# Optimization experiments

Measured on AMD Instinct MI355X. Metric: run time of the kernel, lower is better.

The kernel has to match this reference:

```python
import jax, jax.numpy as jnp
import numpy as np

DIM = 768
H = 12
D = DIM // H  # head_dim = 64
SCALE = D ** -0.5


def _split_heads(x):
    # [b, n, h*d] -> [b, h, n, d]
    b, n, _ = x.shape
    return x.reshape(b, n, H, D).transpose(0, 2, 1, 3)


def setup_inputs() -> dict:
    key = jax.random.key(0)
    ks = jax.random.split(key, 16)
    B, NQ, NKV = 2, 2048, 2048
    w_init = lambda k: jax.random.normal(k, (DIM, DIM), dtype=jnp.float32) * 0.02
    return {
        "words": jax.random.normal(ks[0], (B, NQ, DIM), dtype=jnp.float32),
        "position_words": jax.random.normal(ks[1], (B, NQ, DIM), dtype=jnp.float32),
        "conscious_words": jax.random.normal(ks[2], (B, NQ, DIM), dtype=jnp.float32),
        "cross_kv": jax.random.normal(ks[3], (B, NKV, DIM), dtype=jnp.float32),
        "position_cross": jax.random.normal(ks[4], (B, NKV, DIM), dtype=jnp.float32),
        "Wq_w": w_init(ks[5]), "Wk_w": w_init(ks[6]), "Wv_w": w_init(ks[7]),
        "Wq_p": w_init(ks[8]), "Wk_p": w_init(ks[9]),
        "Wq_c": w_init(ks[10]), "Wk_c": w_init(ks[11]),
        "latent_k": jax.random.normal(ks[12], (DIM,), dtype=jnp.float32),
        "Wo": w_init(ks[13]),
        "bo": jnp.zeros((DIM,), dtype=jnp.float32),
    }


def reference(words, position_words, conscious_words, cross_kv, position_cross,
              Wq_w, Wk_w, Wv_w, Wq_p, Wk_p, Wq_c, Wk_c, latent_k, Wo, bo):
    # Queries from three sources. Sum of the 9 pairwise QK^T scores equals
    # (sum of Qs) @ (sum of Ks)^T by bilinearity of matmul (same math as source).
    q = _split_heads(words @ Wq_w) + _split_heads(position_words @ Wq_p) \
        + _split_heads(conscious_words @ Wq_c)        # [b,h,nq,d]
    # latent conscious key: same vector for every kv position
    kc = (latent_k @ Wk_c).reshape(H, D)              # [h,d]
    k = _split_heads(cross_kv @ Wk_w) + _split_heads(position_cross @ Wk_p) \
        + kc[None, :, None, :]                        # [b,h,nkv,d]
    v = _split_heads(cross_kv @ Wv_w)                 # [b,h,nkv,d]

    score = jnp.einsum('bhid,bhjd->bhij', q, k) * SCALE  # [b,h,nq,nkv]
    attn = jax.nn.softmax(score, axis=-1)
    out = jnp.einsum('bhij,bhjd->bhid', attn, v)      # [b,h,nq,d]
    b, _, nq, _ = out.shape
    out = out.transpose(0, 2, 1, 3).reshape(b, nq, H * D)
    return out @ Wo + bo
```

## Files before the change

### kernel.cpp

```cpp
#include <hip/hip_runtime.h>
#include <math.h>

#define DIM  768
#define NH   12
#define HD   64
#define NQ   2048
#define NKV  2048
#define QSC_LOG2E 0.18033688011112042f

typedef short bf16x8  __attribute__((ext_vector_type(8)));
typedef float f32x4   __attribute__((ext_vector_type(4)));
typedef float f32x16  __attribute__((ext_vector_type(16)));

__device__ __forceinline__ unsigned short f2bf(float f) {
    unsigned u = __float_as_uint(f);
    unsigned r = (u + 0x7FFFu + ((u >> 16) & 1u)) >> 16;
    return (unsigned short)r;
}
__device__ __forceinline__ float bf2f(unsigned short u) {
    return __uint_as_float(((unsigned)u) << 16);
}

__device__ __forceinline__ unsigned cvtpk_bf16(float a, float b) {
    unsigned r;
    asm("v_cvt_pk_bf16_f32 %0, %1, %2" : "=v"(r) : "v"(a), "v"(b));
    return r;
}

__device__ __forceinline__ void plswap(unsigned& a, unsigned& b) {
    asm("v_permlane32_swap_b32 %0, %1" : "+v"(a), "+v"(b));
}

__device__ __forceinline__ float vexp2f(float x) {
#if __has_builtin(__builtin_amdgcn_exp2f)
    return __builtin_amdgcn_exp2f(x);
#else
    float r;
    asm("v_exp_f32 %0, %1\ns_nop 0" : "=v"(r) : "v"(x));
    return r;
#endif
}

__device__ __forceinline__ void ld_lds16(void* lds, const void* g) {
    __builtin_amdgcn_global_load_lds(
        (const __attribute__((address_space(1))) unsigned int*)g,
        (__attribute__((address_space(3))) unsigned int*)lds, 16, 0, 0);
}

__device__ __forceinline__ f32x16 z16() {
    f32x16 r;
    #pragma unroll
    for (int e = 0; e < 16; ++e) r[e] = 0.f;
    return r;
}

union PB16 { unsigned u[4]; bf16x8 v; };

__global__ __launch_bounds__(256)
void prep_kernel(const float* __restrict__ w0, const float* __restrict__ w1,
                 const float* __restrict__ w2, const float* __restrict__ w3,
                 const float* __restrict__ w4, const float* __restrict__ w5,
                 const float* __restrict__ w6, unsigned short* __restrict__ wt,
                 const float* __restrict__ latent, const float* __restrict__ Wkc,
                 float* __restrict__ kc) {
    __shared__ float t[32][33];
    int bid = blockIdx.x;
    if (bid < 4032) {
        int iz = bid / 576, rem = bid - iz * 576;
        int iy = rem / 24, ix = rem - iy * 24;
        const float* Ws[7] = {w0, w1, w2, w3, w4, w5, w6};
        const float* W = Ws[iz];
        unsigned short* D = wt + (size_t)iz * (768 * 768);
        int r0 = iy * 32, c0 = ix * 32;
        int tx = threadIdx.x & 31, ty = threadIdx.x >> 5;
        #pragma unroll
        for (int yy = 0; yy < 4; ++yy)
            t[ty * 4 + yy][tx] = W[(size_t)(r0 + ty * 4 + yy) * 768 + c0 + tx];
        __syncthreads();
        #pragma unroll
        for (int yy = 0; yy < 4; ++yy)
            D[(size_t)(c0 + ty * 4 + yy) * 768 + r0 + tx] = f2bf(t[tx][ty * 4 + yy]);
    } else {
        int jb = bid - 4032;
        float (&red)[16][17] = *reinterpret_cast<float(*)[16][17]>(&t[0][0]);
        int tx = threadIdx.x & 15, ty = threadIdx.x >> 4;
        int j = jb * 16 + tx;
        float acc = 0.f;
        for (int i = ty * 48; i < ty * 48 + 48; ++i)
            acc += latent[i] * Wkc[i * DIM + j];
        red[ty][tx] = acc;
        __syncthreads();
        if (ty == 0) {
            float s = 0.f;
            #pragma unroll
            for (int k = 0; k < 16; ++k) s += red[k][tx];
            kc[j] = s;
        }
    }
}

struct QCfg {
    const float* A0; const float* A1; const float* A2;
    const unsigned short* B0; const unsigned short* B1; const unsigned short* B2;
    const float* bias; float scale; void* out; int npair; int mode;
};

__global__ __launch_bounds__(256)
void gemm_qvk(QCfg c0, QCfg c1, QCfg c2) {
    __shared__ unsigned short As[2][64 * 64];
    __shared__ unsigned short Bs[2][128 * 64];
    const int tid = threadIdx.x;
    const int w = tid >> 6, l = tid & 63, g = l >> 4, r16 = l & 15;

    int p = blockIdx.x;
    int xcd = p & 7, s = p >> 3;
    int bx = s % 6, gg = s / 6;
    int gidx = gg * 8 + xcd;
    int by = gidx & 63, z = gidx >> 6;
    const int n0 = bx * 128, m0 = by * 64;

    QCfg c = (z == 0) ? c0 : (z == 1) ? c1 : c2;
    const float* Alist[3] = {c.A0, c.A1, c.A2};
    const unsigned short* Blist[3] = {c.B0, c.B1, c.B2};

    const int ar = tid >> 2, ac = (tid & 3) * 16;
    const int aswz = (ar & 7) << 4;
    float4 av0, av1, av2, av3;

    f32x4 acc[4][2];
    #pragma unroll
    for (int i = 0; i < 4; ++i)
        #pragma unroll
        for (int j = 0; j < 2; ++j) acc[i][j] = (f32x4){0.f, 0.f, 0.f, 0.f};

#define ALOAD(AP, K0) { \
    const float* _ap = (AP) + (size_t)(m0 + ar) * 768 + (K0) + ac; \
    av0 = *(const float4*)_ap;       av1 = *(const float4*)(_ap + 4); \
    av2 = *(const float4*)(_ap + 8); av3 = *(const float4*)(_ap + 12); }

#define AWRITE(BUFI) { \
    uint4 u0_, u1_; \
    u0_.x = cvtpk_bf16(av0.x, av0.y); u0_.y = cvtpk_bf16(av0.z, av0.w); \
    u0_.z = cvtpk_bf16(av1.x, av1.y); u0_.w = cvtpk_bf16(av1.z, av1.w); \
    u1_.x = cvtpk_bf16(av2.x, av2.y); u1_.y = cvtpk_bf16(av2.z, av2.w); \
    u1_.z = cvtpk_bf16(av3.x, av3.y); u1_.w = cvtpk_bf16(av3.z, av3.w); \
    *(uint4*)((char*)As[BUFI] + ar * 128 + ((2 * ac) ^ aswz)) = u0_; \
    *(uint4*)((char*)As[BUFI] + ar * 128 + ((2 * ac + 16) ^ aswz)) = u1_; }

#define BSTAGE(BUFI, BP, K0) { _Pragma("unroll") \
    for (int is = 0; is < 4; ++is) { \
        int u = is * 256 + tid, r = u >> 3, cc = u & 7; \
        int col = ((cc ^ (r & 7)) << 3); \
        ld_lds16((char*)Bs[BUFI] + is * 4096 + w * 1024, \
                 (BP) + (size_t)(n0 + r) * 768 + (K0) + col); } }

    const int NSTEPS = c.npair * 12;
    int pn = 0, kn = 0;
    ALOAD(Alist[0], 0);
    BSTAGE(0, Blist[0], 0);
    AWRITE(0);
    kn = 64;
    __syncthreads();

    #pragma unroll 1
    for (int st = 0; st < NSTEPS; ++st) {
        int cur = st & 1;
        bool pre = (st + 1 < NSTEPS);
        if (pre) {
            ALOAD(Alist[pn], kn);
            BSTAGE(cur ^ 1, Blist[pn], kn);
        }
        const char* Ab = (const char*)As[cur];
        const char* Bb = (const char*)Bs[cur];
        #pragma unroll
        for (int kk = 0; kk < 2; ++kk) {
            bf16x8 af[4], bf[2];
            #pragma unroll
            for (int i = 0; i < 4; ++i) {
                int row = i * 16 + r16;
                af[i] = *(const bf16x8*)(Ab + row * 128 +
                          ((kk * 64 + g * 16) ^ ((row & 7) << 4)));
            }
            #pragma unroll
            for (int j = 0; j < 2; ++j) {
                int row = w * 32 + j * 16 + r16;
                bf[j] = *(const bf16x8*)(Bb + row * 128 +
                          ((kk * 64 + g * 16) ^ ((row & 7) << 4)));
            }
            #pragma unroll
            for (int i = 0; i < 4; ++i)
                #pragma unroll
                for (int j = 0; j < 2; ++j)
                    acc[i][j] = __builtin_amdgcn_mfma_f32_16x16x32_bf16(
                        af[i], bf[j], acc[i][j], 0, 0, 0);
        }
        if (pre) {
            AWRITE(cur ^ 1);
            kn += 64; if (kn == 768) { kn = 0; ++pn; }
        }
        __syncthreads();
    }
#undef ALOAD
#undef AWRITE
#undef BSTAGE

    const int mode = c.mode;
    #pragma unroll
    for (int i = 0; i < 4; ++i) {
        #pragma unroll
        for (int j = 0; j < 2; ++j) {
            int col = n0 + w * 32 + j * 16 + r16;
            float bv = (mode == 0 && c.bias) ? c.bias[col] : 0.f;
            #pragma unroll
            for (int rr = 0; rr < 4; ++rr) {
                int row = m0 + i * 16 + g * 4 + rr;
                float v = acc[i][j][rr];
                if (mode == 2) v *= c.scale;
                v += bv;
                if (mode == 3) {
                    int bb = row >> 11, q = row & 2047;
                    ((unsigned short*)c.out)[(size_t)(bb * 768 + col) * 2048 + q] = f2bf(v);
                } else {
                    ((unsigned short*)c.out)[(size_t)row * 768 + col] = f2bf(v);
                }
            }
        }
    }
}

__global__ __launch_bounds__(256)
void gemm_out(const unsigned short* __restrict__ A,
              const unsigned short* __restrict__ B,
              const float* __restrict__ bias, float* __restrict__ Cout) {
    __shared__ unsigned short As[2][64 * 64];
    __shared__ unsigned short Bs[2][128 * 64];
    const int tid = threadIdx.x;
    const int w = tid >> 6, l = tid & 63, g = l >> 4, r16 = l & 15;

    int o_lin = blockIdx.x;
    int wl = (o_lin & 7) * 48 + (o_lin >> 3);
    int bx = wl % 6, by = wl / 6;
    const int n0 = bx * 128, m0 = by * 64;

    f32x4 acc[4][2];
    #pragma unroll
    for (int i = 0; i < 4; ++i)
        #pragma unroll
        for (int j = 0; j < 2; ++j) acc[i][j] = (f32x4){0.f, 0.f, 0.f, 0.f};

#define GSTAGE(BUFI, K0) { \
    _Pragma("unroll") \
    for (int is = 0; is < 2; ++is) { \
        int u = is * 256 + tid, r = u >> 3, cc = u & 7; \
        int col = ((cc ^ (r & 7)) << 3); \
        ld_lds16((char*)As[BUFI] + is * 4096 + w * 1024, \
                 A + (size_t)(m0 + r) * 768 + (K0) + col); } \
    _Pragma("unroll") \
    for (int is = 0; is < 4; ++is) { \
        int u = is * 256 + tid, r = u >> 3, cc = u & 7; \
        int col = ((cc ^ (r & 7)) << 3); \
        ld_lds16((char*)Bs[BUFI] + is * 4096 + w * 1024, \
                 B + (size_t)(n0 + r) * 768 + (K0) + col); } }

    GSTAGE(0, 0);
    __syncthreads();

    #pragma unroll 1
    for (int st = 0; st < 12; ++st) {
        int cur = st & 1;
        if (st + 1 < 12) GSTAGE(cur ^ 1, (st + 1) * 64);
        const char* Ab = (const char*)As[cur];
        const char* Bb = (const char*)Bs[cur];
        #pragma unroll
        for (int kk = 0; kk < 2; ++kk) {
            bf16x8 af[4], bf[2];
            #pragma unroll
            for (int i = 0; i < 4; ++i) {
                int row = i * 16 + r16;
                af[i] = *(const bf16x8*)(Ab + row * 128 +
                          ((kk * 64 + g * 16) ^ ((row & 7) << 4)));
            }
            #pragma unroll
            for (int j = 0; j < 2; ++j) {
                int row = w * 32 + j * 16 + r16;
                bf[j] = *(const bf16x8*)(Bb + row * 128 +
                          ((kk * 64 + g * 16) ^ ((row & 7) << 4)));
            }
            #pragma unroll
            for (int i = 0; i < 4; ++i)
                #pragma unroll
                for (int j = 0; j < 2; ++j)
                    acc[i][j] = __builtin_amdgcn_mfma_f32_16x16x32_bf16(
                        af[i], bf[j], acc[i][j], 0, 0, 0);
        }
        __syncthreads();
    }
#undef GSTAGE

    #pragma unroll
    for (int i = 0; i < 4; ++i) {
        #pragma unroll
        for (int j = 0; j < 2; ++j) {
            int col = n0 + w * 32 + j * 16 + r16;
            float bv = bias[col];
            #pragma unroll
            for (int rr = 0; rr < 4; ++rr) {
                int row = m0 + i * 16 + g * 4 + rr;
                Cout[(size_t)row * 768 + col] = acc[i][j][rr] + bv;
            }
        }
    }
}

__global__ __launch_bounds__(256)
void flash2(const unsigned short* __restrict__ Qb,
            const unsigned short* __restrict__ Kb,
            const unsigned short* __restrict__ Vt,
            unsigned short* __restrict__ P0, unsigned short* __restrict__ P1,
            unsigned short* __restrict__ P2, unsigned short* __restrict__ P3,
            float2* __restrict__ ML) {
    __shared__ unsigned short KV[2][2][4096];
    const int tid = threadIdx.x;
    const int w = tid >> 6, l = tid & 63, lo = l & 31, hi = l >> 5;

    int p = blockIdx.x + 64 * blockIdx.y;
    int xcd = p & 7, s = p >> 3;
    int gg = s >> 6, inner = s & 63;
    int bh = gg * 8 + xcd;
    int qi = inner >> 2, part = inner & 3;
    int b = bh / NH, h = bh % NH;
    int q0 = qi * 128;
    int kvbase = part * 512;

    bf16x8 qf[4];
    {
        const unsigned short* Qrow =
            Qb + (size_t)(b * NQ + q0 + w * 32 + lo) * DIM + h * HD + hi * 8;
        #pragma unroll
        for (int kc = 0; kc < 4; ++kc) qf[kc] = *(const bf16x8*)(Qrow + kc * 16);
    }

    f32x16 o0 = z16(), o1 = z16();
    float m = -3.0e38f, lsum = 0.f;

    const unsigned short* Kbase = Kb + (size_t)(b * NKV) * DIM + h * HD;
    const unsigned short* Vbase = Vt + ((size_t)b * DIM + h * HD) * NKV;

#define FSTAGE(BUFI, T0) { \
    _Pragma("unroll") \
    for (int is = 0; is < 2; ++is) { \
        int u = is * 256 + tid, r = u >> 3, cc = u & 7; \
        int col = ((cc ^ (r & 7)) << 3); \
        ld_lds16((char*)KV[BUFI][0] + is * 4096 + w * 1024, \
                 Kbase + (size_t)((T0) + r) * 768 + col); \
        ld_lds16((char*)KV[BUFI][1] + is * 4096 + w * 1024, \
                 Vbase + (size_t)r * 2048 + (T0) + col); } }

    FSTAGE(0, kvbase);
    __syncthreads();

    #pragma unroll 1
    for (int t = 0; t < 8; ++t) {
        int cur = t & 1;
        if (t < 7) FSTAGE(cur ^ 1, kvbase + (t + 1) * 64);

        const char* Kp = (const char*)KV[cur][0];
        const char* Vp = (const char*)KV[cur][1];

        f32x16 s0 = z16(), s1 = z16();
        __builtin_amdgcn_s_setprio(1);
        #pragma unroll
        for (int kc = 0; kc < 4; ++kc) {
            int r0 = lo, r1 = 32 + lo;
            bf16x8 k0 = *(const bf16x8*)(Kp + r0 * 128 +
                          ((kc * 32 + hi * 16) ^ ((r0 & 7) << 4)));
            bf16x8 k1 = *(const bf16x8*)(Kp + r1 * 128 +
                          ((kc * 32 + hi * 16) ^ ((r1 & 7) << 4)));
            s0 = __builtin_amdgcn_mfma_f32_32x32x16_bf16(k0, qf[kc], s0, 0, 0, 0);
            s1 = __builtin_amdgcn_mfma_f32_32x32x16_bf16(k1, qf[kc], s1, 0, 0, 0);
        }
        __builtin_amdgcn_s_setprio(0);

        float a8[8];
        #pragma unroll
        for (int e = 0; e < 8; ++e)
            a8[e] = fmaxf(fmaxf(fmaxf(s0[e], s0[e + 8]), s1[e]), s1[e + 8]);
        float pm = fmaxf(fmaxf(fmaxf(fmaxf(a8[0], a8[1]), fmaxf(a8[2], a8[3])),
                               fmaxf(fmaxf(a8[4], a8[5]), fmaxf(a8[6], a8[7]))), -3.0e38f);
        pm = fmaxf(pm, __shfl_xor(pm, 32));

        if (__any(pm > m + 10.f)) {
            float mn = fmaxf(m, pm);
            float sc = vexp2f(m - mn);
            lsum *= sc;
            #pragma unroll
            for (int e = 0; e < 16; ++e) { o0[e] *= sc; o1[e] *= sc; }
            m = mn;
        }

        #pragma unroll
        for (int e = 0; e < 16; ++e) {
            s0[e] = vexp2f(s0[e] - m);
            s1[e] = vexp2f(s1[e] - m);
        }

        float b8[8];
        #pragma unroll
        for (int e = 0; e < 8; ++e)
            b8[e] = (s0[e] + s0[e + 8]) + (s1[e] + s1[e + 8]);
        float rs = ((b8[0] + b8[1]) + (b8[2] + b8[3])) +
                   ((b8[4] + b8[5]) + (b8[6] + b8[7]));
        rs += __shfl_xor(rs, 32);
        lsum += rs;

        PB16 pb[4];
        #pragma unroll
        for (int cc = 0; cc < 2; ++cc) {
            unsigned a0 = cvtpk_bf16(s0[cc * 8 + 0], s0[cc * 8 + 1]);
            unsigned a1 = cvtpk_bf16(s0[cc * 8 + 2], s0[cc * 8 + 3]);
            unsigned b0 = cvtpk_bf16(s0[cc * 8 + 4], s0[cc * 8 + 5]);
            unsigned b1 = cvtpk_bf16(s0[cc * 8 + 6], s0[cc * 8 + 7]);
            plswap(a0, b0);
            plswap(a1, b1);
            pb[cc].u[0] = a0; pb[cc].u[1] = a1; pb[cc].u[2] = b0; pb[cc].u[3] = b1;
            unsigned c0 = cvtpk_bf16(s1[cc * 8 + 0], s1[cc * 8 + 1]);
            unsigned c1 = cvtpk_bf16(s1[cc * 8 + 2], s1[cc * 8 + 3]);
            unsigned d0 = cvtpk_bf16(s1[cc * 8 + 4], s1[cc * 8 + 5]);
            unsigned d1 = cvtpk_bf16(s1[cc * 8 + 6], s1[cc * 8 + 7]);
            plswap(c0, d0);
            plswap(c1, d1);
            pb[2 + cc].u[0] = c0; pb[2 + cc].u[1] = c1;
            pb[2 + cc].u[2] = d0; pb[2 + cc].u[3] = d1;
        }

        __builtin_amdgcn_s_setprio(1);
        #pragma unroll
        for (int c = 0; c < 4; ++c) {
            int r0 = lo, r1 = 32 + lo;
            bf16x8 v0 = *(const bf16x8*)(Vp + r0 * 128 +
                          ((c * 32 + hi * 16) ^ ((r0 & 7) << 4)));
            bf16x8 v1 = *(const bf16x8*)(Vp + r1 * 128 +
                          ((c * 32 + hi * 16) ^ ((r1 & 7) << 4)));
            o0 = __builtin_amdgcn_mfma_f32_32x32x16_bf16(v0, pb[c].v, o0, 0, 0, 0);
            o1 = __builtin_amdgcn_mfma_f32_32x32x16_bf16(v1, pb[c].v, o1, 0, 0, 0);
        }
        __builtin_amdgcn_s_setprio(0);
        __syncthreads();
    }
#undef FSTAGE

    unsigned short* Pp = (part == 0) ? P0 : (part == 1) ? P1 : (part == 2) ? P2 : P3;
    const int q = q0 + w * 32 + lo;
    unsigned short* Op = Pp + ((size_t)bh * 2048 + q) * 64;
    #pragma unroll
    for (int grp = 0; grp < 4; ++grp) {
        int r0 = grp * 4;
        int d0 = grp * 8 + 4 * hi;
        uint2 v0, v1;
        v0.x = cvtpk_bf16(o0[r0 + 0], o0[r0 + 1]);
        v0.y = cvtpk_bf16(o0[r0 + 2], o0[r0 + 3]);
        *(uint2*)(Op + d0) = v0;
        v1.x = cvtpk_bf16(o1[r0 + 0], o1[r0 + 1]);
        v1.y = cvtpk_bf16(o1[r0 + 2], o1[r0 + 3]);
        *(uint2*)(Op + 32 + d0) = v1;
    }
    if (hi == 0)
        ML[(size_t)(part * 24 + bh) * 2048 + q] = make_float2(m, lsum);
}

__global__ __launch_bounds__(256)
void combine4(const unsigned short* __restrict__ P0, const unsigned short* __restrict__ P1,
              const unsigned short* __restrict__ P2, const unsigned short* __restrict__ P3,
              const float2* __restrict__ ML, unsigned short* __restrict__ AO) {
    int bh = blockIdx.y;
    int idx = blockIdx.x * 256 + threadIdx.x;
    int q = idx >> 1, dh = (idx & 1) * 32;

    float2 u0 = ML[(size_t)(0 * 24 + bh) * 2048 + q];
    float2 u1 = ML[(size_t)(1 * 24 + bh) * 2048 + q];
    float2 u2 = ML[(size_t)(2 * 24 + bh) * 2048 + q];
    float2 u3 = ML[(size_t)(3 * 24 + bh) * 2048 + q];
    float M = fmaxf(fmaxf(u0.x, u1.x), fmaxf(u2.x, u3.x));
    float w0 = vexp2f(u0.x - M), w1 = vexp2f(u1.x - M);
    float w2 = vexp2f(u2.x - M), w3 = vexp2f(u3.x - M);
    float inv = 1.f / (w0 * u0.y + w1 * u1.y + w2 * u2.y + w3 * u3.y);
    w0 *= inv; w1 *= inv; w2 *= inv; w3 *= inv;

    size_t off = ((size_t)bh * 2048 + q) * 64 + dh;
    float acc[32];
    #pragma unroll
    for (int e = 0; e < 32; ++e) acc[e] = 0.f;
    const unsigned short* Ps[4] = {P0, P1, P2, P3};
    float ws[4] = {w0, w1, w2, w3};
    #pragma unroll
    for (int pp = 0; pp < 4; ++pp) {
        const unsigned short* src = Ps[pp] + off;
        float wv = ws[pp];
        #pragma unroll
        for (int c = 0; c < 4; ++c) {
            ushort4 hh2;
            uint4 vv = *(const uint4*)(src + c * 8);
            unsigned uu[4] = {vv.x, vv.y, vv.z, vv.w};
            #pragma unroll
            for (int e = 0; e < 4; ++e) {
                acc[c * 8 + e * 2 + 0] += wv * bf2f((unsigned short)(uu[e] & 0xFFFF));
                acc[c * 8 + e * 2 + 1] += wv * bf2f((unsigned short)(uu[e] >> 16));
            }
            (void)hh2;
        }
    }
    int b = bh / NH, h = bh % NH;
    unsigned short* dst = AO + ((size_t)(b * 2048 + q)) * DIM + h * HD + dh;
    #pragma unroll
    for (int c = 0; c < 4; ++c) {
        uint4 ov;
        ov.x = cvtpk_bf16(acc[c * 8 + 0], acc[c * 8 + 1]);
        ov.y = cvtpk_bf16(acc[c * 8 + 2], acc[c * 8 + 3]);
        ov.z = cvtpk_bf16(acc[c * 8 + 4], acc[c * 8 + 5]);
        ov.w = cvtpk_bf16(acc[c * 8 + 6], acc[c * 8 + 7]);
        *(uint4*)(dst + c * 8) = ov;
    }
}

extern "C" void kernel_launch(void* const* d_in, const int* in_sizes, int n_in,
                              void* d_out, int out_size, void* d_ws, size_t ws_size,
                              hipStream_t stream) {
    const float* words   = (const float*)d_in[0];
    const float* posw    = (const float*)d_in[1];
    const float* consc   = (const float*)d_in[2];
    const float* cross   = (const float*)d_in[3];
    const float* pcross  = (const float*)d_in[4];
    const float* Wq_w    = (const float*)d_in[5];
    const float* Wk_w    = (const float*)d_in[6];
    const float* Wv_w    = (const float*)d_in[7];
    const float* Wq_p    = (const float*)d_in[8];
    const float* Wk_p    = (const float*)d_in[9];
    const float* Wq_c    = (const float*)d_in[10];
    const float* Wk_c    = (const float*)d_in[11];
    const float* latentk = (const float*)d_in[12];
    const float* Wo      = (const float*)d_in[13];
    const float* bo      = (const float*)d_in[14];

    char* arena = (char*)d_ws;
    const size_t WTE = 768 * 768;
    unsigned short* WT = (unsigned short*)(arena);
    unsigned short* QB = (unsigned short*)(arena + 8257536);
    unsigned short* VT = (unsigned short*)(arena + 14548992);
    unsigned short* KB = (unsigned short*)(arena + 20840448);
    unsigned short* P0 = (unsigned short*)(arena + 27131904);
    unsigned short* P1 = (unsigned short*)(arena + 33423360);
    unsigned short* P2 = (unsigned short*)(arena + 39714816);
    unsigned short* P3 = (unsigned short*)(arena);
    float2* ML         = (float2*)(arena + 46006272);
    float* KCV         = (float*)(arena + 47579136);

    prep_kernel<<<dim3(4080), dim3(256), 0, stream>>>(
        Wq_w, Wq_p, Wq_c, Wk_w, Wk_p, Wv_w, Wo, WT, latentk, Wk_c, KCV);

    QCfg cq = { words, posw, consc,
                WT + 0 * WTE, WT + 1 * WTE, WT + 2 * WTE,
                nullptr, QSC_LOG2E, QB, 3, 2 };
    QCfg cv = { cross, nullptr, nullptr,
                WT + 5 * WTE, nullptr, nullptr,
                nullptr, 1.f, VT, 1, 3 };
    QCfg ck = { cross, pcross, nullptr,
                WT + 3 * WTE, WT + 4 * WTE, nullptr,
                KCV, 1.f, KB, 2, 0 };
    gemm_qvk<<<dim3(1152), dim3(256), 0, stream>>>(cq, cv, ck);

    flash2<<<dim3(64, 24), dim3(256), 0, stream>>>(QB, KB, VT, P0, P1, P2, P3, ML);

    combine4<<<dim3(16, 24), dim3(256), 0, stream>>>(P0, P1, P2, P3, ML, QB);

    gemm_out<<<dim3(384), dim3(256), 0, stream>>>(QB, WT + 6 * WTE, bo, (float*)d_out);
}
```

Baseline: 140.0 us.

## Pre-convert activations to bf16 and enlarge QKV GEMM tiles to 128x128

The prep kernel now also converts words, position_words and cross_kv to bf16 in the workspace. The fused QKV GEMM then streams those activations straight into LDS with async loads, and only the last fp32 pair is register-prefetched and converted. The GEMM tile grows from 64x128 to 128x128 with a 2x2 wave layout, which halves the block count and raises operand reuse. Buffering drops from double to single with explicit waitcnt barriers, and the transposed V output is written as packed stores. In exchange it adds an extra global round trip for the converted activations, reshuffles the workspace layout, and exposes less load latency because LDS is no longer double-buffered.

```diff
diff --git a/kernel.cpp b/kernel.cpp
--- a/kernel.cpp
+++ b/kernel.cpp
@@ -62,7 +62,9 @@
                  const float* __restrict__ w4, const float* __restrict__ w5,
                  const float* __restrict__ w6, unsigned short* __restrict__ wt,
                  const float* __restrict__ latent, const float* __restrict__ Wkc,
-                 float* __restrict__ kc) {
+                 float* __restrict__ kc,
+                 const float* __restrict__ cwords, const float* __restrict__ cposw,
+                 const float* __restrict__ ccross, unsigned short* __restrict__ Sbase) {
     __shared__ float t[32][33];
     int bid = blockIdx.x;
     if (bid < 4032) {
@@ -80,7 +82,7 @@
         #pragma unroll
         for (int yy = 0; yy < 4; ++yy)
             D[(size_t)(c0 + ty * 4 + yy) * 768 + r0 + tx] = f2bf(t[tx][ty * 4 + yy]);
-    } else {
+    } else if (bid < 4080) {
         int jb = bid - 4032;
         float (&red)[16][17] = *reinterpret_cast<float(*)[16][17]>(&t[0][0]);
         int tx = threadIdx.x & 15, ty = threadIdx.x >> 4;
@@ -96,132 +98,178 @@
             for (int k = 0; k < 16; ++k) s += red[k][tx];
             kc[j] = s;
         }
+    } else {
+        int cvt = bid - 4080;
+        int ti = cvt / 1536, blk = cvt - ti * 1536;
+        const float* srcs[3] = {cwords, cposw, ccross};
+        const float* src = srcs[ti];
+        unsigned short* dst = Sbase + (size_t)ti * 3145728;
+        size_t i = ((size_t)blk * 256 + threadIdx.x) * 8;
+        float4 f0 = *(const float4*)(src + i);
+        float4 f1 = *(const float4*)(src + i + 4);
+        uint4 o;
+        o.x = cvtpk_bf16(f0.x, f0.y); o.y = cvtpk_bf16(f0.z, f0.w);
+        o.z = cvtpk_bf16(f1.x, f1.y); o.w = cvtpk_bf16(f1.z, f1.w);
+        *(uint4*)(dst + i) = o;
     }
 }
 
 struct QCfg {
-    const float* A0; const float* A1; const float* A2;
+    const unsigned short* Ab0; const unsigned short* Ab1;
+    const float* Afp;
     const unsigned short* B0; const unsigned short* B1; const unsigned short* B2;
-    const float* bias; float scale; void* out; int npair; int mode;
+    const float* bias; float scale; void* out; int npair; int fppair; int mode;
 };
 
 __global__ __launch_bounds__(256)
 void gemm_qvk(QCfg c0, QCfg c1, QCfg c2) {
-    __shared__ unsigned short As[2][64 * 64];
-    __shared__ unsigned short Bs[2][128 * 64];
+    __shared__ unsigned short As[128 * 64];
+    __shared__ unsigned short Bs[128 * 64];
     const int tid = threadIdx.x;
     const int w = tid >> 6, l = tid & 63, g = l >> 4, r16 = l & 15;
+    const int wr = w >> 1, wc = w & 1;
 
     int p = blockIdx.x;
     int xcd = p & 7, s = p >> 3;
     int bx = s % 6, gg = s / 6;
     int gidx = gg * 8 + xcd;
-    int by = gidx & 63, z = gidx >> 6;
-    const int n0 = bx * 128, m0 = by * 64;
+    int by = gidx & 31, z = gidx >> 5;
+    const int n0 = bx * 128, m0 = by * 128;
 
     QCfg c = (z == 0) ? c0 : (z == 1) ? c1 : c2;
-    const float* Alist[3] = {c.A0, c.A1, c.A2};
-    const unsigned short* Blist[3] = {c.B0, c.B1, c.B2};
-
-    const int ar = tid >> 2, ac = (tid & 3) * 16;
-    const int aswz = (ar & 7) << 4;
-    float4 av0, av1, av2, av3;
-
-    f32x4 acc[4][2];
+    const unsigned short* Abf[2] = {c.Ab0, c.Ab1};
+    const unsigned short* Bl[3] = {c.B0, c.B1, c.B2};
+
+    const int arf = tid >> 1, acf = (tid & 1) * 32;
+    const int aswz = (arf & 7) << 4;
+
+    f32x4 acc[4][4];
     #pragma unroll
     for (int i = 0; i < 4; ++i)
         #pragma unroll
-        for (int j = 0; j < 2; ++j) acc[i][j] = (f32x4){0.f, 0.f, 0.f, 0.f};
-
-#define ALOAD(AP, K0) { \
-    const float* _ap = (AP) + (size_t)(m0 + ar) * 768 + (K0) + ac; \
-    av0 = *(const float4*)_ap;       av1 = *(const float4*)(_ap + 4); \
-    av2 = *(const float4*)(_ap + 8); av3 = *(const float4*)(_ap + 12); }
-
-#define AWRITE(BUFI) { \
-    uint4 u0_, u1_; \
-    u0_.x = cvtpk_bf16(av0.x, av0.y); u0_.y = cvtpk_bf16(av0.z, av0.w); \
-    u0_.z = cvtpk_bf16(av1.x, av1.y); u0_.w = cvtpk_bf16(av1.z, av1.w); \
-    u1_.x = cvtpk_bf16(av2.x, av2.y); u1_.y = cvtpk_bf16(av2.z, av2.w); \
-    u1_.z = cvtpk_bf16(av3.x, av3.y); u1_.w = cvtpk_bf16(av3.z, av3.w); \
-    *(uint4*)((char*)As[BUFI] + ar * 128 + ((2 * ac) ^ aswz)) = u0_; \
-    *(uint4*)((char*)As[BUFI] + ar * 128 + ((2 * ac + 16) ^ aswz)) = u1_; }
-
-#define BSTAGE(BUFI, BP, K0) { _Pragma("unroll") \
-    for (int is = 0; is < 4; ++is) { \
-        int u = is * 256 + tid, r = u >> 3, cc = u & 7; \
-        int col = ((cc ^ (r & 7)) << 3); \
-        ld_lds16((char*)Bs[BUFI] + is * 4096 + w * 1024, \
-                 (BP) + (size_t)(n0 + r) * 768 + (K0) + col); } }
+        for (int j = 0; j < 4; ++j) acc[i][j] = (f32x4){0.f, 0.f, 0.f, 0.f};
+
+    float4 x0, x1, x2, x3, x4, x5, x6, x7;
+    float4 y0, y1, y2, y3, y4, y5, y6, y7;
+
+#define ALOAD8(p0, p1, p2, p3, p4, p5, p6, p7, KC) { \
+    const float* _ap = c.Afp + (size_t)(m0 + arf) * 768 + (KC) + acf; \
+    p0 = *(const float4*)(_ap + 0);  p1 = *(const float4*)(_ap + 4); \
+    p2 = *(const float4*)(_ap + 8);  p3 = *(const float4*)(_ap + 12); \
+    p4 = *(const float4*)(_ap + 16); p5 = *(const float4*)(_ap + 20); \
+    p6 = *(const float4*)(_ap + 24); p7 = *(const float4*)(_ap + 28); }
+#define AWR8(v0, v1, v2, v3, v4, v5, v6, v7) { uint4 u0_, u1_, u2_, u3_; \
+    u0_.x = cvtpk_bf16(v0.x, v0.y); u0_.y = cvtpk_bf16(v0.z, v0.w); \
+    u0_.z = cvtpk_bf16(v1.x, v1.y); u0_.w = cvtpk_bf16(v1.z, v1.w); \
+    u1_.x = cvtpk_bf16(v2.x, v2.y); u1_.y = cvtpk_bf16(v2.z, v2.w); \
+    u1_.z = cvtpk_bf16(v3.x, v3.y); u1_.w = cvtpk_bf16(v3.z, v3.w); \
+    u2_.x = cvtpk_bf16(v4.x, v4.y); u2_.y = cvtpk_bf16(v4.z, v4.w); \
+    u2_.z = cvtpk_bf16(v5.x, v5.y); u2_.w = cvtpk_bf16(v5.z, v5.w); \
+    u3_.x = cvtpk_bf16(v6.x, v6.y); u3_.y = cvtpk_bf16(v6.z, v6.w); \
+    u3_.z = cvtpk_bf16(v7.x, v7.y); u3_.w = cvtpk_bf16(v7.z, v7.w); \
+    char* _dst = (char*)As + arf * 128; \
+    *(uint4*)(_dst + ((2 * acf + 0)  ^ aswz)) = u0_; \
+    *(uint4*)(_dst + ((2 * acf + 16) ^ aswz)) = u1_; \
+    *(uint4*)(_dst + ((2 * acf + 32) ^ aswz)) = u2_; \
+    *(uint4*)(_dst + ((2 * acf + 48) ^ aswz)) = u3_; }
+#define BARA  asm volatile("s_barrier" ::: "memory")
+#define BARB8 asm volatile("s_waitcnt vmcnt(8)\ns_waitcnt lgkmcnt(0)\ns_barrier" ::: "memory")
+#define BARB0 asm volatile("s_waitcnt vmcnt(0)\ns_waitcnt lgkmcnt(0)\ns_barrier" ::: "memory")
 
     const int NSTEPS = c.npair * 12;
     int pn = 0, kn = 0;
-    ALOAD(Alist[0], 0);
-    BSTAGE(0, Blist[0], 0);
-    AWRITE(0);
-    kn = 64;
-    __syncthreads();
+    bool f = false;
 
     #pragma unroll 1
     for (int st = 0; st < NSTEPS; ++st) {
-        int cur = st & 1;
-        bool pre = (st + 1 < NSTEPS);
-        if (pre) {
-            ALOAD(Alist[pn], kn);
-            BSTAGE(cur ^ 1, Blist[pn], kn);
-        }
-        const char* Ab = (const char*)As[cur];
-        const char* Bb = (const char*)Bs[cur];
+        int knN = kn + 64, pnN = pn;
+        if (knN == 768) { knN = 0; ++pnN; }
+        const bool fnext = (st + 1 < NSTEPS) && (pnN == c.fppair);
+
+        BARA;
+        if (f) {
+            if (st & 1) { AWR8(y0, y1, y2, y3, y4, y5, y6, y7); }
+            else        { AWR8(x0, x1, x2, x3, x4, x5, x6, x7); }
+        } else {
+            const unsigned short* Ap = Abf[pn];
+            #pragma unroll
+            for (int is = 0; is < 4; ++is) {
+                int u = is * 256 + tid, r = u >> 3, cc2 = u & 7;
+                int col = ((cc2 ^ (r & 7)) << 3);
+                ld_lds16((char*)As + is * 4096 + w * 1024,
+                         Ap + (size_t)(m0 + r) * 768 + kn + col);
+            }
+        }
+        {
+            const unsigned short* Bp = Bl[pn];
+            #pragma unroll
+            for (int is = 0; is < 4; ++is) {
+                int u = is * 256 + tid, r = u >> 3, cc2 = u & 7;
+                int col = ((cc2 ^ (r & 7)) << 3);
+                ld_lds16((char*)Bs + is * 4096 + w * 1024,
+                         Bp + (size_t)(n0 + r) * 768 + kn + col);
+            }
+        }
+        if (fnext) {
+            if ((st + 1) & 1) { ALOAD8(y0, y1, y2, y3, y4, y5, y6, y7, knN); }
+            else              { ALOAD8(x0, x1, x2, x3, x4, x5, x6, x7, knN); }
+            BARB8;
+        } else {
+            BARB0;
+        }
+
         #pragma unroll
         for (int kk = 0; kk < 2; ++kk) {
-            bf16x8 af[4], bf[2];
+            bf16x8 af[4], bf[4];
             #pragma unroll
             for (int i = 0; i < 4; ++i) {
-                int row = i * 16 + r16;
-                af[i] = *(const bf16x8*)(Ab + row * 128 +
+                int row = wr * 64 + i * 16 + r16;
+                af[i] = *(const bf16x8*)((const char*)As + row * 128 +
                           ((kk * 64 + g * 16) ^ ((row & 7) << 4)));
             }
             #pragma unroll
-            for (int j = 0; j < 2; ++j) {
-                int row = w * 32 + j * 16 + r16;
-                bf[j] = *(const bf16x8*)(Bb + row * 128 +
+            for (int j = 0; j < 4; ++j) {
+                int row = wc * 64 + j * 16 + r16;
+                bf[j] = *(const bf16x8*)((const char*)Bs + row * 128 +
                           ((kk * 64 + g * 16) ^ ((row & 7) << 4)));
             }
             #pragma unroll
             for (int i = 0; i < 4; ++i)
                 #pragma unroll
-                for (int j = 0; j < 2; ++j)
+                for (int j = 0; j < 4; ++j)
                     acc[i][j] = __builtin_amdgcn_mfma_f32_16x16x32_bf16(
                         af[i], bf[j], acc[i][j], 0, 0, 0);
         }
-        if (pre) {
-            AWRITE(cur ^ 1);
-            kn += 64; if (kn == 768) { kn = 0; ++pn; }
-        }
-        __syncthreads();
-    }
-#undef ALOAD
-#undef AWRITE
-#undef BSTAGE
+        kn = knN; pn = pnN; f = fnext;
+    }
+#undef ALOAD8
+#undef AWR8
+#undef BARA
+#undef BARB8
+#undef BARB0
 
     const int mode = c.mode;
     #pragma unroll
     for (int i = 0; i < 4; ++i) {
         #pragma unroll
-        for (int j = 0; j < 2; ++j) {
-            int col = n0 + w * 32 + j * 16 + r16;
-            float bv = (mode == 0 && c.bias) ? c.bias[col] : 0.f;
-            #pragma unroll
-            for (int rr = 0; rr < 4; ++rr) {
-                int row = m0 + i * 16 + g * 4 + rr;
-                float v = acc[i][j][rr];
-                if (mode == 2) v *= c.scale;
-                v += bv;
-                if (mode == 3) {
-                    int bb = row >> 11, q = row & 2047;
-                    ((unsigned short*)c.out)[(size_t)(bb * 768 + col) * 2048 + q] = f2bf(v);
-                } else {
-                    ((unsigned short*)c.out)[(size_t)row * 768 + col] = f2bf(v);
+        for (int j = 0; j < 4; ++j) {
+            int col = n0 + wc * 64 + j * 16 + r16;
+            int row0 = m0 + wr * 64 + i * 16 + g * 4;
+            if (mode == 3) {
+                int bb = row0 >> 11, q = row0 & 2047;
+                uint2 v;
+                v.x = cvtpk_bf16(acc[i][j][0], acc[i][j][1]);
+                v.y = cvtpk_bf16(acc[i][j][2], acc[i][j][3]);
+                *(uint2*)((unsigned short*)c.out +
+                          (size_t)(bb * 768 + col) * 2048 + q) = v;
+            } else {
+                float bv = (mode == 0 && c.bias) ? c.bias[col] : 0.f;
+                #pragma unroll
+                for (int rr = 0; rr < 4; ++rr) {
+                    float v = acc[i][j][rr];
+                    if (mode == 2) v *= c.scale;
+                    v += bv;
+                    ((unsigned short*)c.out)[(size_t)(row0 + rr) * 768 + col] = f2bf(v);
                 }
             }
         }
@@ -385,8 +433,8 @@
         #pragma unroll
         for (int e = 0; e < 8; ++e)
             a8[e] = fmaxf(fmaxf(fmaxf(s0[e], s0[e + 8]), s1[e]), s1[e + 8]);
-        float pm = fmaxf(fmaxf(fmaxf(fmaxf(a8[0], a8[1]), fmaxf(a8[2], a8[3])),
-                               fmaxf(fmaxf(a8[4], a8[5]), fmaxf(a8[6], a8[7]))), -3.0e38f);
+        float pm = fmaxf(fmaxf(fmaxf(a8[0], a8[1]), fmaxf(a8[2], a8[3])),
+                         fmaxf(fmaxf(a8[4], a8[5]), fmaxf(a8[6], a8[7])));
         pm = fmaxf(pm, __shfl_xor(pm, 32));
 
         if (__any(pm > m + 10.f)) {
@@ -498,7 +546,6 @@
         float wv = ws[pp];
         #pragma unroll
         for (int c = 0; c < 4; ++c) {
-            ushort4 hh2;
             uint4 vv = *(const uint4*)(src + c * 8);
             unsigned uu[4] = {vv.x, vv.y, vv.z, vv.w};
             #pragma unroll
@@ -506,7 +553,6 @@
                 acc[c * 8 + e * 2 + 0] += wv * bf2f((unsigned short)(uu[e] & 0xFFFF));
                 acc[c * 8 + e * 2 + 1] += wv * bf2f((unsigned short)(uu[e] >> 16));
             }
-            (void)hh2;
         }
     }
     int b = bh / NH, h = bh % NH;
@@ -543,30 +589,31 @@
 
     char* arena = (char*)d_ws;
     const size_t WTE = 768 * 768;
-    unsigned short* WT = (unsigned short*)(arena);
-    unsigned short* QB = (unsigned short*)(arena + 8257536);
-    unsigned short* VT = (unsigned short*)(arena + 14548992);
-    unsigned short* KB = (unsigned short*)(arena + 20840448);
-    unsigned short* P0 = (unsigned short*)(arena + 27131904);
-    unsigned short* P1 = (unsigned short*)(arena + 33423360);
-    unsigned short* P2 = (unsigned short*)(arena + 39714816);
-    unsigned short* P3 = (unsigned short*)(arena);
+    unsigned short* S0 = (unsigned short*)(arena);
+    unsigned short* S1 = (unsigned short*)(arena +  6291456);
+    unsigned short* S2 = (unsigned short*)(arena + 12582912);
+    unsigned short* KB = (unsigned short*)(arena + 18874368);
+    unsigned short* WT = (unsigned short*)(arena + 25165824);
+    unsigned short* P3 = (unsigned short*)(arena + 25165824);
+    unsigned short* QB = (unsigned short*)(arena + 33423360);
+    unsigned short* VT = (unsigned short*)(arena + 39714816);
     float2* ML         = (float2*)(arena + 46006272);
     float* KCV         = (float*)(arena + 47579136);
-
-    prep_kernel<<<dim3(4080), dim3(256), 0, stream>>>(
-        Wq_w, Wq_p, Wq_c, Wk_w, Wk_p, Wv_w, Wo, WT, latentk, Wk_c, KCV);
-
-    QCfg cq = { words, posw, consc,
-                WT + 0 * WTE, WT + 1 * WTE, WT + 2 * WTE,
-                nullptr, QSC_LOG2E, QB, 3, 2 };
-    QCfg cv = { cross, nullptr, nullptr,
-                WT + 5 * WTE, nullptr, nullptr,
-                nullptr, 1.f, VT, 1, 3 };
-    QCfg ck = { cross, pcross, nullptr,
-                WT + 3 * WTE, WT + 4 * WTE, nullptr,
-                KCV, 1.f, KB, 2, 0 };
-    gemm_qvk<<<dim3(1152), dim3(256), 0, stream>>>(cq, cv, ck);
+    unsigned short* P0 = S0;
+    unsigned short* P1 = S1;
+    unsigned short* P2 = S2;
+
+    prep_kernel<<<dim3(8688), dim3(256), 0, stream>>>(
+        Wq_w, Wq_p, Wq_c, Wk_w, Wk_p, Wv_w, Wo, WT, latentk, Wk_c, KCV,
+        words, posw, cross, S0);
+
+    QCfg cq = { S0, S1, consc, WT + 0 * WTE, WT + 1 * WTE, WT + 2 * WTE,
+                nullptr, QSC_LOG2E, QB, 3, 2, 2 };
+    QCfg cv = { S2, nullptr, nullptr, WT + 5 * WTE, nullptr, nullptr,
+                nullptr, 1.f, VT, 1, -1, 3 };
+    QCfg ck = { S2, nullptr, pcross, WT + 3 * WTE, WT + 4 * WTE, nullptr,
+                KCV, 1.f, KB, 2, 1, 0 };
+    gemm_qvk<<<dim3(576), dim3(256), 0, stream>>>(cq, cv, ck);
 
     flash2<<<dim3(64, 24), dim3(256), 0, stream>>>(QB, KB, VT, P0, P1, P2, P3, ML);
 
```

After: 158.4 us. +13.2%, slower.
